# Performance work log

Hardware: AMD Instinct MI355X
Metric: run time of the kernel (lower is better)

The kernel has to match this reference:

```python
import jax, jax.numpy as jnp
import numpy as np
import math

B, T, D, NH, HD = 2, 1024, 768, 12, 64
V, L, E, CAP_F, H = 50257, 2, 8, 1.25, 2048
AUX_W, Z_W, THETA, EPS = 0.01, 0.001, 10000.0, 1e-5
N = B * T
CAP = int(math.ceil(N / E * CAP_F))  # 320


def setup_inputs():
    key = jax.random.key(0)
    ks = jax.random.split(key, 8)
    s = 0.02
    return dict(
        idx=jax.random.randint(ks[0], (B, T), 0, V),
        wte=jax.random.normal(ks[1], (V, D), jnp.float32) * s,
        wqkv=jax.random.normal(ks[2], (L, D, 3 * D), jnp.float32) * s,
        q_norm_w=jnp.ones((L, D), jnp.float32),
        k_norm_w=jnp.ones((L, D), jnp.float32),
        o_proj=jax.random.normal(ks[3], (L, D, D), jnp.float32) * s,
        ffn_norm_w=jnp.ones((L, D), jnp.float32),
        gate_w=jax.random.normal(ks[4], (L, D, E), jnp.float32) * s,
        w13=jax.random.normal(ks[5], (L, E, D, 2 * H), jnp.float32) * s,
        w2=jax.random.normal(ks[6], (L, E, H, D), jnp.float32) * s,
        ln_f_w=jnp.ones((D,), jnp.float32),
    )


def rmsnorm(x, w):
    return x * jax.lax.rsqrt(jnp.mean(x * x, axis=-1, keepdims=True) + EPS) * w


def rope(x, cos, sin):
    # x: (B, nh, T, HD) viewed as complex pairs on last dim
    xr = x.reshape(*x.shape[:-1], HD // 2, 2)
    x0, x1 = xr[..., 0], xr[..., 1]
    out = jnp.stack([x0 * cos - x1 * sin, x0 * sin + x1 * cos], axis=-1)
    return out.reshape(x.shape)


def moe(x, gate_w, w13, w2):
    # x: (B, T, D) -> Switch MoE (k=1) with capacity CAP and token drops
    x_flat = x.reshape(N, D).astype(jnp.float32)
    logits = x_flat @ gate_w  # (N, E) fp32
    probs = jax.nn.softmax(logits, axis=-1)
    top = jnp.argmax(logits, axis=-1)  # (N,)
    prob_mass = probs.mean(axis=0)
    fraction = jax.nn.one_hot(top, E, dtype=jnp.float32).mean(axis=0)
    balance_loss = jnp.sum(prob_mass * fraction) * AUX_W * E
    z = jax.nn.logsumexp(logits, axis=-1)
    z_loss = jnp.mean(z * z) * Z_W
    aux = balance_loss + z_loss

    sort_idx = jnp.argsort(top)  # stable
    sorted_assign = top[sort_idx]
    counts = jnp.bincount(sorted_assign, length=E)
    offsets = jnp.concatenate([jnp.zeros((1,), counts.dtype), jnp.cumsum(counts)])[:E]
    rank = jnp.arange(N) - offsets[sorted_assign]  # position within expert segment
    keep = rank < CAP
    x_perm = x_flat[sort_idx]
    slot = jnp.where(keep, rank, CAP)  # dropped -> overflow slot
    buf = jnp.zeros((E, CAP + 1, D), jnp.float32).at[sorted_assign, slot].set(x_perm)
    xb = buf[:, :CAP]  # (E, CAP, D)
    gu = jnp.einsum('ecd,edh->ech', xb, w13)  # (E, CAP, 2H)
    g, u = jnp.split(gu, 2, axis=-1)
    y = jnp.einsum('ech,ehd->ecd', jax.nn.silu(g) * u, w2)  # (E, CAP, D)
    out_perm = y[sorted_assign, jnp.minimum(rank, CAP - 1)] * keep[:, None]
    out_flat = jnp.zeros((N, D), jnp.float32).at[sort_idx].set(out_perm)
    return out_flat.reshape(B, T, D), aux, top.reshape(B, T), keep[jnp.argsort(sort_idx)].reshape(B, T)


def forward(idx, wte, wqkv, q_norm_w, k_norm_w, o_proj, ffn_norm_w, gate_w, w13, w2, ln_f_w):
    x = wte[idx]  # (B, T, D)
    freqs = 1.0 / (THETA ** (jnp.arange(0, HD, 2, dtype=jnp.float32) / HD))
    ang = jnp.outer(jnp.arange(T, dtype=jnp.float32), freqs)  # (T, HD//2)
    cos, sin = jnp.cos(ang)[None, None], jnp.sin(ang)[None, None]
    mask = jnp.where(jnp.tril(jnp.ones((T, T), bool)), 0.0, -jnp.inf)
    aux_total = jnp.float32(0.0)
    for l in range(L):
        qkv = x @ wqkv[l]
        q, k, v = jnp.split(qkv, 3, axis=-1)
        q = rmsnorm(q, q_norm_w[l])
        k = rmsnorm(k, k_norm_w[l])
        q = q.reshape(B, T, NH, HD).transpose(0, 2, 1, 3)
        k = k.reshape(B, T, NH, HD).transpose(0, 2, 1, 3)
        v = v.reshape(B, T, NH, HD).transpose(0, 2, 1, 3)
        q, k = rope(q, cos, sin), rope(k, cos, sin)
        scores = jnp.einsum('bhqd,bhkd->bhqk', q, k) / math.sqrt(HD) + mask
        attn = jax.nn.softmax(scores, axis=-1)
        y = jnp.einsum('bhqk,bhkd->bhqd', attn, v).transpose(0, 2, 1, 3).reshape(B, T, D)
        h = x + y @ o_proj[l]
        ffn_in = rmsnorm(h, ffn_norm_w[l])
        moe_out, aux, _, _ = moe(ffn_in, gate_w[l], w13[l], w2[l])
        aux_total = aux_total + aux
        x = h + moe_out
    x = rmsnorm(x, ln_f_w)
    logits = x @ wte.T  # tied lm_head
    return logits, aux_total


def reference(idx, wte, wqkv, q_norm_w, k_norm_w, o_proj, ffn_norm_w, gate_w, w13, w2, ln_f_w):
    return forward(idx, wte, wqkv, q_norm_w, k_norm_w, o_proj, ffn_norm_w, gate_w, w13, w2, ln_f_w)
```

## Files before the change

### kernel.cpp

```cpp
#include <hip/hip_runtime.h>

typedef __attribute__((ext_vector_type(8))) _Float16 half8;
typedef __attribute__((ext_vector_type(4))) float f32x4;

constexpr int Bc = 2, Tc = 1024, Dc = 768, NHc = 12, HDc = 64;
constexpr int Vc = 50257, Lc = 2, Ec = 8, Hc = 2048;
constexpr int Ntok = Bc * Tc;
constexpr int CAPc = 320, CAPPc = 384;
constexpr long long LOGITS_N = (long long)Bc * Tc * Vc;

typedef const __attribute__((address_space(1))) unsigned int* gas_t;
typedef __attribute__((address_space(3))) unsigned int* las_t;
__device__ __forceinline__ void gload16(const void* g, void* l) {
  __builtin_amdgcn_global_load_lds((gas_t)g, (las_t)l, 16, 0, 0);
}

__device__ __forceinline__ void splitf16(float a, unsigned short& h, unsigned short& l) {
  _Float16 hh = (_Float16)a;
  _Float16 ll = (_Float16)(a - (float)hh);
  h = __builtin_bit_cast(unsigned short, hh);
  l = __builtin_bit_cast(unsigned short, ll);
}
__device__ __forceinline__ unsigned short f16o(float a) {
  _Float16 hh = (_Float16)a;
  return __builtin_bit_cast(unsigned short, hh);
}


__global__ void embed_k(const int* __restrict__ idx, const float* __restrict__ wte,
                        float* __restrict__ x, unsigned short* __restrict__ x16,
                        float* __restrict__ psum, float* __restrict__ z2) {
  int n = blockIdx.x;
  int t = threadIdx.x;
  if (n == 0) {
    if (t < Lc * Ec) psum[t] = 0.f;
    if (t >= 32 && t < 32 + Lc) z2[t - 32] = 0.f;
  }
  long long v = idx[n];
  const float4* src = (const float4*)(wte + v * 768);
  float4* dst = (float4*)(x + (long long)n * 768);
  if (t < 192) {
    float4 val = src[t];
    dst[t] = val;
    ushort4 h, l;
    splitf16(val.x, h.x, l.x); splitf16(val.y, h.y, l.y);
    splitf16(val.z, h.z, l.z); splitf16(val.w, h.w, l.w);
    unsigned short* d = x16 + (long long)n * 1536 + t * 4;
    *(ushort4*)d = h;
    *(ushort4*)(d + 768) = l;
  }
}

__global__ void f2h4(const float* __restrict__ in, unsigned short* __restrict__ out,
                     long long n4) {
  long long i = (long long)blockIdx.x * 256 + threadIdx.x;
  if (i >= n4) return;
  float4 v = ((const float4*)in)[i];
  ushort4 o;
  o.x = f16o(v.x); o.y = f16o(v.y); o.z = f16o(v.z); o.w = f16o(v.w);
  ((ushort4*)out)[i] = o;
}

template <int SP, int ILV>
__global__ void __launch_bounds__(256) split2_wT(const float* __restrict__ src,
    unsigned short* __restrict__ dst, int K, int N, long long sS, long long sD) {
  __shared__ float t[32][33];
  int z = blockIdx.z;
  src += (long long)z * sS;
  dst += (long long)z * sD;
  int n0 = blockIdx.x * 32, k0 = blockIdx.y * 32;
  int tid = threadIdx.x;
  int r = tid >> 3, c4 = (tid & 7) * 4;
  float4 v = *(const float4*)(src + (long long)(k0 + r) * N + n0 + c4);
  t[r][c4 + 0] = v.x; t[r][c4 + 1] = v.y; t[r][c4 + 2] = v.z; t[r][c4 + 3] = v.w;
  __syncthreads();
  int n = tid >> 3, kq = (tid & 7) * 4;
  ushort4 h, l;
  splitf16(t[kq + 0][n], h.x, l.x);
  splitf16(t[kq + 1][n], h.y, l.y);
  splitf16(t[kq + 2][n], h.z, l.z);
  splitf16(t[kq + 3][n], h.w, l.w);
  const int lda = SP ? 2 * K : K;
  int nd = n0 + n;
  if (ILV) {
    int hh = nd & 2047, iu = nd >> 11;
    nd = ((hh >> 4) << 5) + (iu << 4) + (hh & 15);
  }
  unsigned short* d = dst + (long long)nd * lda + k0 + kq;
  *(ushort4*)d = h;
  if (SP) *(ushort4*)(d + K) = l;
}

__global__ void __launch_bounds__(256) rmsnorm_k(const float* in, int istride,
                                                 float* outp, int ostride,
                                                 const float* w) {
  long long n = blockIdx.x;
  const float* xr = in + n * istride;
  float* yr = outp + n * ostride;
  int tid = threadIdx.x;
  float s = 0.f;
  for (int i = tid; i < 768; i += 256) { float v = xr[i]; s += v * v; }
  #pragma unroll
  for (int o = 32; o; o >>= 1) s += __shfl_down(s, o);
  __shared__ float red[4];
  __shared__ float bs;
  if ((tid & 63) == 0) red[tid >> 6] = s;
  __syncthreads();
  if (tid == 0) bs = rsqrtf((red[0] + red[1] + red[2] + red[3]) / 768.0f + 1e-5f);
  __syncthreads();
  float sc = bs;
  for (int i = tid; i < 768; i += 256) yr[i] = xr[i] * sc * w[i];
}

__global__ void __launch_bounds__(256) rmsnorm_h(const float* in,
                                                 unsigned short* outp, const float* w) {
  long long n = blockIdx.x;
  const float* xr = in + n * 768;
  unsigned short* yr = outp + n * 768;
  int tid = threadIdx.x;
  float s = 0.f;
  for (int i = tid; i < 768; i += 256) { float v = xr[i]; s += v * v; }
  #pragma unroll
  for (int o = 32; o; o >>= 1) s += __shfl_down(s, o);
  __shared__ float red[4];
  __shared__ float bs;
  if ((tid & 63) == 0) red[tid >> 6] = s;
  __syncthreads();
  if (tid == 0) bs = rsqrtf((red[0] + red[1] + red[2] + red[3]) / 768.0f + 1e-5f);
  __syncthreads();
  float sc = bs;
  for (int i = tid; i < 768; i += 256) yr[i] = f16o(xr[i] * sc * w[i]);
}

__global__ void __launch_bounds__(256) qk_rope(const float* __restrict__ qkv,
    const float* __restrict__ qnw, const float* __restrict__ knw,
    unsigned short* __restrict__ qr, unsigned short* __restrict__ kr,
    unsigned short* __restrict__ vr) {
  int n = blockIdx.x;
  int t = n & 1023, b = n >> 10;
  const float* row = qkv + (long long)n * 2304;
  int tid = threadIdx.x;
  float sq = 0.f, sk = 0.f;
  for (int i = tid; i < 768; i += 256) {
    float q = row[i]; sq += q * q;
    float k = row[768 + i]; sk += k * k;
  }
  #pragma unroll
  for (int o = 32; o; o >>= 1) { sq += __shfl_down(sq, o); sk += __shfl_down(sk, o); }
  __shared__ float redq[4], redk[4];
  __shared__ float bq, bk;
  if ((tid & 63) == 0) { redq[tid >> 6] = sq; redk[tid >> 6] = sk; }
  __syncthreads();
  if (tid == 0) {
    bq = rsqrtf((redq[0] + redq[1] + redq[2] + redq[3]) / 768.0f + 1e-5f);
    bk = rsqrtf((redk[0] + redk[1] + redk[2] + redk[3]) / 768.0f + 1e-5f);
  }
  __syncthreads();
  float nq = bq, nk = bk;
  for (int i = tid; i < 384; i += 256) {
    int hh = i >> 5, j = i & 31;
    int c = hh * 64 + 2 * j;
    float ang = (float)t * powf(10000.0f, -((float)j * (1.0f / 32.0f)));
    float cs = cosf(ang), sn = sinf(ang);
    int z = b * 12 + hh;
    long long qb = ((long long)z * 1024 + t) * 128 + 2 * j;
    unsigned short h0, l0, h1, l1;
    float q0 = row[c] * nq * qnw[c], q1 = row[c + 1] * nq * qnw[c + 1];
    splitf16(q0 * cs - q1 * sn, h0, l0);
    splitf16(q0 * sn + q1 * cs, h1, l1);
    *(unsigned int*)&qr[qb] = (unsigned)h0 | ((unsigned)h1 << 16);
    *(unsigned int*)&qr[qb + 64] = (unsigned)l0 | ((unsigned)l1 << 16);
    float k0 = row[768 + c] * nk * knw[c], k1 = row[768 + c + 1] * nk * knw[c + 1];
    splitf16(k0 * cs - k1 * sn, h0, l0);
    splitf16(k0 * sn + k1 * cs, h1, l1);
    *(unsigned int*)&kr[qb] = (unsigned)h0 | ((unsigned)h1 << 16);
    *(unsigned int*)&kr[qb + 64] = (unsigned)l0 | ((unsigned)l1 << 16);
    splitf16(row[1536 + c], h0, l0);
    splitf16(row[1536 + c + 1], h1, l1);
    long long vb = ((long long)z * 64 + 2 * j) * 2048 + t;
    vr[vb] = h0; vr[vb + 1024] = l0;
    vr[vb + 2048] = h1; vr[vb + 3072] = l1;
  }
}

__global__ void __launch_bounds__(256) flash_attn(
    const unsigned short* __restrict__ qr, const unsigned short* __restrict__ kr,
    const unsigned short* __restrict__ vr, unsigned short* __restrict__ yout) {
  __shared__ __align__(16) unsigned short Ph[4][16][72];
  __shared__ __align__(16) unsigned short Pl[4][16][72];
  int bid = blockIdx.x;
  int z = bid >> 4;
  int qt = 15 - (bid & 15);
  int b = z / 12, h = z % 12;
  int q0 = qt * 64;
  int wave = threadIdx.x >> 6, lane = threadIdx.x & 63;
  int lr = lane & 15, lg = lane >> 4;
  int qw = q0 + wave * 16;
  half8 af[2][2];
  const unsigned short* qbase = qr + ((long long)z * 1024 + qw + lr) * 128;
  #pragma unroll
  for (int ks = 0; ks < 2; ++ks)
    #pragma unroll
    for (int p = 0; p < 2; ++p)
      af[ks][p] = *(const half8*)(qbase + p * 64 + ks * 32 + lg * 8);
  f32x4 accy[4];
  #pragma unroll
  for (int df = 0; df < 4; ++df) accy[df] = (f32x4){0.f, 0.f, 0.f, 0.f};
  float mrun[4] = {-3.4e38f, -3.4e38f, -3.4e38f, -3.4e38f};
  float srun[4] = {0.f, 0.f, 0.f, 0.f};
  for (int kt = 0; kt <= qt; ++kt) {
    int kv0 = kt * 64;
    f32x4 s[4];
    #pragma unroll
    for (int nf = 0; nf < 4; ++nf) s[nf] = (f32x4){0.f, 0.f, 0.f, 0.f};
    const unsigned short* kbase = kr + ((long long)z * 1024 + kv0 + lr) * 128;
    #pragma unroll
    for (int nf = 0; nf < 4; ++nf) {
      const unsigned short* kb = kbase + nf * 16 * 128;
      #pragma unroll
      for (int ks = 0; ks < 2; ++ks) {
        half8 bh = *(const half8*)(kb + ks * 32 + lg * 8);
        half8 bl = *(const half8*)(kb + 64 + ks * 32 + lg * 8);
        s[nf] = __builtin_amdgcn_mfma_f32_16x16x32_f16(af[ks][0], bh, s[nf], 0, 0, 0);
        s[nf] = __builtin_amdgcn_mfma_f32_16x16x32_f16(af[ks][1], bh, s[nf], 0, 0, 0);
        s[nf] = __builtin_amdgcn_mfma_f32_16x16x32_f16(af[ks][0], bl, s[nf], 0, 0, 0);
      }
    }
    bool diag = (kt == qt);
    #pragma unroll
    for (int nf = 0; nf < 4; ++nf)
      #pragma unroll
      for (int j = 0; j < 4; ++j) {
        float v = s[nf][j] * 0.125f;
        if (diag && (nf * 16 + lr > wave * 16 + lg * 4 + j)) v = -1e30f;
        s[nf][j] = v;
      }
    #pragma unroll
    for (int j = 0; j < 4; ++j) {
      float tm = fmaxf(fmaxf(s[0][j], s[1][j]), fmaxf(s[2][j], s[3][j]));
      #pragma unroll
      for (int o = 1; o < 16; o <<= 1) tm = fmaxf(tm, __shfl_xor(tm, o));
      float mnew = fmaxf(mrun[j], tm);
      float sc = expf(mrun[j] - mnew);
      float ts = 0.f;
      #pragma unroll
      for (int nf = 0; nf < 4; ++nf) {
        float p = expf(s[nf][j] - mnew);
        ts += p;
        unsigned short ph, pl;
        splitf16(p, ph, pl);
        Ph[wave][lg * 4 + j][nf * 16 + lr] = ph;
        Pl[wave][lg * 4 + j][nf * 16 + lr] = pl;
      }
      #pragma unroll
      for (int o = 1; o < 16; o <<= 1) ts += __shfl_xor(ts, o);
      srun[j] = srun[j] * sc + ts;
      mrun[j] = mnew;
      #pragma unroll
      for (int df = 0; df < 4; ++df) accy[df][j] *= sc;
    }
    #pragma unroll
    for (int ks2 = 0; ks2 < 2; ++ks2) {
      half8 aph = *(const half8*)&Ph[wave][lr][ks2 * 32 + lg * 8];
      half8 apl = *(const half8*)&Pl[wave][lr][ks2 * 32 + lg * 8];
      #pragma unroll
      for (int df = 0; df < 4; ++df) {
        const unsigned short* vb =
            vr + ((long long)z * 64 + df * 16 + lr) * 2048 + kv0 + ks2 * 32 + lg * 8;
        half8 bvh = *(const half8*)vb;
        half8 bvl = *(const half8*)(vb + 1024);
        accy[df] = __builtin_amdgcn_mfma_f32_16x16x32_f16(aph, bvh, accy[df], 0, 0, 0);
        accy[df] = __builtin_amdgcn_mfma_f32_16x16x32_f16(apl, bvh, accy[df], 0, 0, 0);
        accy[df] = __builtin_amdgcn_mfma_f32_16x16x32_f16(aph, bvl, accy[df], 0, 0, 0);
      }
    }
  }
  float inv[4];
  #pragma unroll
  for (int j = 0; j < 4; ++j) inv[j] = 1.0f / srun[j];
  #pragma unroll
  for (int df = 0; df < 4; ++df)
    #pragma unroll
    for (int j = 0; j < 4; ++j) {
      long long tok = (long long)b * 1024 + qw + lg * 4 + j;
      int col = h * 64 + df * 16 + lr;
      unsigned short hh, ll;
      splitf16(accy[df][j] * inv[j], hh, ll);
      yout[tok * 1536 + col] = hh;
      yout[tok * 1536 + 768 + col] = ll;
    }
}

__global__ void __launch_bounds__(256) gate_k(const float* __restrict__ xin,
    const float* __restrict__ gw, int* __restrict__ top,
    float* __restrict__ psum, float* __restrict__ z2) {
  __shared__ float gws[768 * 8];
  __shared__ float pacc[8];
  __shared__ float zacc;
  int tid = threadIdx.x;
  for (int i = tid; i < 768 * 8 / 4; i += 256) ((float4*)gws)[i] = ((const float4*)gw)[i];
  if (tid < 8) pacc[tid] = 0.f;
  if (tid == 0) zacc = 0.f;
  __syncthreads();
  int n = blockIdx.x * 256 + tid;
  const float4* xr4 = (const float4*)(xin + (long long)n * 768);
  float l[8] = {0, 0, 0, 0, 0, 0, 0, 0};
  for (int d4 = 0; d4 < 192; ++d4) {
    float4 xv = xr4[d4];
    const float* g = &gws[d4 * 32];
    #pragma unroll
    for (int e = 0; e < 8; ++e)
      l[e] += xv.x * g[e] + xv.y * g[8 + e] + xv.z * g[16 + e] + xv.w * g[24 + e];
  }
  float mx = l[0]; int bi = 0;
  #pragma unroll
  for (int e = 1; e < 8; ++e) if (l[e] > mx) { mx = l[e]; bi = e; }
  float p[8]; float se = 0.f;
  #pragma unroll
  for (int e = 0; e < 8; ++e) { p[e] = expf(l[e] - mx); se += p[e]; }
  float z = mx + logf(se);
  top[n] = bi;
  #pragma unroll
  for (int e = 0; e < 8; ++e) atomicAdd(&pacc[e], p[e] / se);
  atomicAdd(&zacc, z * z);
  __syncthreads();
  if (tid < 8) atomicAdd(&psum[tid], pacc[tid]);
  if (tid == 0) atomicAdd(z2, zacc);
}

__global__ void route_scan(const int* __restrict__ top, int* __restrict__ rank,
                           int* __restrict__ cnt) {
  int lane = threadIdx.x;
  int c[8] = {0, 0, 0, 0, 0, 0, 0, 0};
  unsigned long long below = (1ull << lane) - 1ull;
  for (int s = 0; s < Ntok / 64; ++s) {
    int n = s * 64 + lane;
    int e = top[n];
    int r = 0;
    #pragma unroll
    for (int q = 0; q < 8; ++q) {
      unsigned long long m = __ballot(e == q);
      if (e == q) r = c[q] + __popcll(m & below);
      c[q] += __popcll(m);
    }
    rank[n] = r;
  }
  #pragma unroll
  for (int q = 0; q < 8; ++q) if (lane == q) cnt[q] = c[q];
}

template <int SP>
__global__ void scatter_xb(const float* __restrict__ xin, const int* __restrict__ top,
                           const int* __restrict__ rank, unsigned short* __restrict__ xb) {
  int n = blockIdx.x;
  int r = rank[n];
  if (r >= CAPc) return;
  int e = top[n];
  int t = threadIdx.x;
  if (t >= 192) return;
  float4 v = ((const float4*)(xin + (long long)n * 768))[t];
  ushort4 h, l;
  splitf16(v.x, h.x, l.x); splitf16(v.y, h.y, l.y);
  splitf16(v.z, h.z, l.z); splitf16(v.w, h.w, l.w);
  const int lda = SP ? 1536 : 768;
  unsigned short* dst = xb + ((long long)e * CAPPc + r) * lda + t * 4;
  *(ushort4*)dst = h;
  if (SP) *(ushort4*)(dst + 768) = l;
}

__global__ void gather_add(const float* __restrict__ h, const float* __restrict__ yexp,
                           const int* __restrict__ top, const int* __restrict__ rank,
                           float* __restrict__ xo, unsigned short* __restrict__ x16) {
  int n = blockIdx.x;
  int r = rank[n], e = top[n];
  bool kept = r < CAPc;
  int rc = kept ? r : (CAPc - 1);
  const float4* hs = (const float4*)(h + (long long)n * 768);
  const float4* ys = (const float4*)(yexp + ((long long)e * CAPPc + rc) * 768);
  float4* dst = (float4*)(xo + (long long)n * 768);
  int t = threadIdx.x;
  if (t < 192) {
    float4 v = hs[t];
    if (kept) { float4 y = ys[t]; v.x += y.x; v.y += y.y; v.z += y.z; v.w += y.w; }
    dst[t] = v;
    ushort4 hh, ll;
    splitf16(v.x, hh.x, ll.x); splitf16(v.y, hh.y, ll.y);
    splitf16(v.z, hh.z, ll.z); splitf16(v.w, hh.w, ll.w);
    unsigned short* d = x16 + (long long)n * 1536 + t * 4;
    *(ushort4*)d = hh;
    *(ushort4*)(d + 768) = ll;
  }
}

__global__ void aux_fin(const float* __restrict__ psum, const int* __restrict__ cnt,
                        const float* __restrict__ z2, float* __restrict__ outp) {
  if (threadIdx.x == 0) {
    float aux = 0.f;
    for (int l = 0; l < Lc; ++l) {
      float bl = 0.f;
      for (int e = 0; e < 8; ++e)
        bl += (psum[l * 8 + e] * (1.0f / 2048.0f)) * ((float)cnt[l * 8 + e] * (1.0f / 2048.0f));
      aux += bl * (0.01f * 8.0f) + (z2[l] * (1.0f / 2048.0f)) * 0.001f;
    }
    outp[0] = aux;
  }
}

template <int BN, int SPLIT, int ADD, int NTAIL, int SILU>
__global__ void __launch_bounds__(256) gemm_h(
    const unsigned short* __restrict__ A, const unsigned short* __restrict__ Bt,
    float* __restrict__ C, const float* __restrict__ Add,
    int M, int N, int K, int ldc, int gx, int gy,
    long long sA, long long sB, int zdiv, long long sC1, long long sC2) {
  constexpr int FN = (BN == 128) ? 4 : 2;
  constexpr int APL = 128 * 32;
  constexpr int BPL = BN * 32;
  constexpr int BUF = 2 * APL + 2 * BPL;
  __shared__ __align__(16) unsigned short lds[2][BUF];
  int tot = gridDim.x;
  int lin = blockIdx.x;
  if ((tot & 7) == 0) lin = (lin & 7) * (tot >> 3) + (lin >> 3);
  int pz = lin / (gx * gy);
  int r2 = lin - pz * (gx * gy);
  const int m0 = (r2 % gx) * 128, n0 = (r2 / gx) * BN;
  A += (long long)pz * sA;
  Bt += (long long)pz * sB;
  const long long co = (long long)(pz / zdiv) * sC1 + (long long)(pz % zdiv) * sC2;
  const int lda = SPLIT ? 2 * K : K;
  const int NS = SPLIT ? K / 32 : K / 64;
  const int tid = threadIdx.x;
  const int lane = tid & 63, wave = tid >> 6;
  const int wm = (BN == 128) ? (wave >> 1) : (wave & 1);
  const int wn = (BN == 128) ? (wave & 1) : (wave >> 1);
  const int srow = tid >> 2, scol = (tid & 3) * 8;
  const unsigned short* Ar = A + (long long)(m0 + srow) * lda + scol;
  int br0 = n0 + srow;
  if (NTAIL) br0 = min(br0, N - 1);
  const unsigned short* Br = Bt + (long long)br0 * lda + scol;
  int br1 = n0 + srow + 64;
  if (NTAIL) br1 = min(br1, N - 1);
  const unsigned short* Br2 = Bt + (long long)br1 * lda + scol;

  auto STAGE = [&](int buf, int s) {
    const int kh = SPLIT ? s * 32 : s * 64;
    const int kl = SPLIT ? K + s * 32 : s * 64 + 32;
    unsigned short* L = lds[buf];
    gload16(Ar + kh, &L[wave * 512]);
    gload16(Ar + (long long)64 * lda + kh, &L[2048 + wave * 512]);
    gload16(Ar + kl, &L[APL + wave * 512]);
    gload16(Ar + (long long)64 * lda + kl, &L[APL + 2048 + wave * 512]);
    gload16(Br + kh, &L[2 * APL + wave * 512]);
    gload16(Br + kl, &L[2 * APL + BPL + wave * 512]);
    if (BN == 128) {
      gload16(Br2 + kh, &L[2 * APL + 2048 + wave * 512]);
      gload16(Br2 + kl, &L[2 * APL + BPL + 2048 + wave * 512]);
    }
  };

  f32x4 acc[4][FN];
  #pragma unroll
  for (int m = 0; m < 4; ++m)
    #pragma unroll
    for (int n = 0; n < FN; ++n) acc[m][n] = (f32x4){0.f, 0.f, 0.f, 0.f};

  STAGE(0, 0);
  int cur = 0;
  for (int s = 0; s < NS; ++s) {
    asm volatile("s_waitcnt vmcnt(0)" ::: "memory");
    __builtin_amdgcn_sched_barrier(0);
    __builtin_amdgcn_s_barrier();
    if (s + 1 < NS) STAGE(cur ^ 1, s + 1);
    const unsigned short* L = lds[cur];
    half8 bfh[FN], bfl[FN];
    #pragma unroll
    for (int n = 0; n < FN; ++n) {
      int bo = (wn * (FN * 16) + n * 16 + (lane & 15)) * 32 + (lane >> 4) * 8;
      bfh[n] = *(const half8*)&L[2 * APL + bo];
      bfl[n] = *(const half8*)&L[2 * APL + BPL + bo];
    }
    __builtin_amdgcn_s_setprio(1);
    #pragma unroll
    for (int m = 0; m < 4; ++m) {
      int ao = (wm * 64 + m * 16 + (lane & 15)) * 32 + (lane >> 4) * 8;
      half8 afh = *(const half8*)&L[ao];
      half8 afl = *(const half8*)&L[APL + ao];
      #pragma unroll
      for (int n = 0; n < FN; ++n) {
        acc[m][n] = __builtin_amdgcn_mfma_f32_16x16x32_f16(afh, bfh[n], acc[m][n], 0, 0, 0);
        if (SPLIT) {
          acc[m][n] = __builtin_amdgcn_mfma_f32_16x16x32_f16(afl, bfh[n], acc[m][n], 0, 0, 0);
          acc[m][n] = __builtin_amdgcn_mfma_f32_16x16x32_f16(afh, bfl[n], acc[m][n], 0, 0, 0);
        } else {
          acc[m][n] = __builtin_amdgcn_mfma_f32_16x16x32_f16(afl, bfl[n], acc[m][n], 0, 0, 0);
        }
      }
    }
    __builtin_amdgcn_s_setprio(0);
    cur ^= 1;
  }
  if constexpr (SILU) {
    unsigned short* act = (unsigned short*)C;
    #pragma unroll
    for (int m = 0; m < 4; ++m)
      #pragma unroll
      for (int p = 0; p < FN / 2; ++p) {
        f32x4 g = acc[m][2 * p], u = acc[m][2 * p + 1];
        int colh = ((n0 + wn * (FN * 16)) >> 1) + p * 16 + (lane & 15);
        #pragma unroll
        for (int j = 0; j < 4; ++j) {
          long long row = m0 + wm * 64 + m * 16 + (lane >> 4) * 4 + j;
          float gv = g[j];
          float a = gv / (1.f + expf(-gv)) * u[j];
          long long o = co + row * ldc + colh;
          if (SILU == 1) {
            unsigned short hh, ll;
            splitf16(a, hh, ll);
            act[o] = hh;
            act[o + 2048] = ll;
          } else {
            act[o] = f16o(a);
          }
        }
      }
  } else {
    #pragma unroll
    for (int m = 0; m < 4; ++m)
      #pragma unroll
      for (int n = 0; n < FN; ++n) {
        int col = n0 + wn * (FN * 16) + n * 16 + (lane & 15);
        if (!NTAIL || col < N) {
          #pragma unroll
          for (int j = 0; j < 4; ++j) {
            long long row = m0 + wm * 64 + m * 16 + (lane >> 4) * 4 + j;
            long long o = co + row * ldc + col;
            float v = acc[m][n][j];
            if (ADD) v += Add[o];
            C[o] = v;
          }
        }
      }
  }
}

__global__ void __launch_bounds__(512) gemm_logits(
    const unsigned short* __restrict__ A, const unsigned short* __restrict__ Bt,
    float* __restrict__ C, int M, int N, int K, int ldc, int gx) {
  constexpr int BUFS = 24576;
  constexpr int BOFF = 16384;
  __shared__ __align__(16) unsigned short lds[3 * BUFS];
  int tot = gridDim.x;
  int lin = blockIdx.x;
  if ((tot & 7) == 0) lin = (lin & 7) * (tot >> 3) + (lin >> 3);
  const int m0 = (lin % gx) * 256, n0 = (lin / gx) * 128;
  const int tid = threadIdx.x;
  const int lane = tid & 63;
  const int wm = (tid >> 6) >> 1, wn = (tid >> 6) & 1;
  const int NS = K / 64;

  auto STAGE = [&](int buf, int t) {
    const int k0 = t * 64;
    unsigned short* L = lds + buf * BUFS;
    #pragma unroll
    for (int i = 0; i < 4; ++i) {
      int idx = tid + i * 512;
      int row = idx >> 3, blk = idx & 7;
      gload16(A + (long long)(m0 + row) * K + k0 + ((blk ^ (row & 7)) << 3),
              L + idx * 8);
    }
    #pragma unroll
    for (int i = 0; i < 2; ++i) {
      int idx = tid + i * 512;
      int row = idx >> 3, blk = idx & 7;
      int br = min(n0 + row, N - 1);
      gload16(Bt + (long long)br * K + k0 + ((blk ^ (row & 7)) << 3),
              L + BOFF + idx * 8);
    }
  };

  f32x4 acc[4][4];
  #pragma unroll
  for (int mf = 0; mf < 4; ++mf)
    #pragma unroll
    for (int nf = 0; nf < 4; ++nf) acc[mf][nf] = (f32x4){0.f, 0.f, 0.f, 0.f};

  STAGE(0, 0); STAGE(1, 1);
  for (int s = 0; s < NS; ++s) {
    if (s + 1 < NS) asm volatile("s_waitcnt vmcnt(6)" ::: "memory");
    else            asm volatile("s_waitcnt vmcnt(0)" ::: "memory");
    __builtin_amdgcn_sched_barrier(0);
    __builtin_amdgcn_s_barrier();
    if (s + 2 < NS) STAGE((s + 2) % 3, s + 2);
    const unsigned short* L = lds + (s % 3) * BUFS;
    half8 a[4][2], b[4][2];
    #pragma unroll
    for (int mf = 0; mf < 4; ++mf)
      #pragma unroll
      for (int ks = 0; ks < 2; ++ks) {
        int row = wm * 64 + mf * 16 + (lane & 15);
        int blk = (ks * 4 + (lane >> 4)) ^ (row & 7);
        a[mf][ks] = *(const half8*)(L + row * 64 + blk * 8);
      }
    #pragma unroll
    for (int nf = 0; nf < 4; ++nf)
      #pragma unroll
      for (int ks = 0; ks < 2; ++ks) {
        int row = wn * 64 + nf * 16 + (lane & 15);
        int blk = (ks * 4 + (lane >> 4)) ^ (row & 7);
        b[nf][ks] = *(const half8*)(L + BOFF + row * 64 + blk * 8);
      }
    __builtin_amdgcn_s_setprio(1);
    #pragma unroll
    for (int ks = 0; ks < 2; ++ks)
      #pragma unroll
      for (int mf = 0; mf < 4; ++mf)
        #pragma unroll
        for (int nf = 0; nf < 4; ++nf)
          acc[mf][nf] = __builtin_amdgcn_mfma_f32_16x16x32_f16(a[mf][ks], b[nf][ks],
                                                               acc[mf][nf], 0, 0, 0);
    __builtin_amdgcn_s_setprio(0);
  }
  #pragma unroll
  for (int mf = 0; mf < 4; ++mf)
    #pragma unroll
    for (int nf = 0; nf < 4; ++nf) {
      int col = n0 + wn * 64 + nf * 16 + (lane & 15);
      if (col < N) {
        #pragma unroll
        for (int j = 0; j < 4; ++j) {
          long long row = m0 + wm * 64 + mf * 16 + (lane >> 4) * 4 + j;
          C[row * (long long)ldc + col] = acc[mf][nf][j];
        }
      }
    }
}


extern "C" void kernel_launch(void* const* d_in, const int* in_sizes, int n_in,
                              void* d_out, int out_size, void* d_ws, size_t ws_size,
                              hipStream_t stream) {
  (void)in_sizes; (void)n_in; (void)out_size; (void)ws_size;
  const int*   idx   = (const int*)d_in[0];
  const float* wte   = (const float*)d_in[1];
  const float* wqkv  = (const float*)d_in[2];
  const float* qnw   = (const float*)d_in[3];
  const float* knw   = (const float*)d_in[4];
  const float* oproj = (const float*)d_in[5];
  const float* ffnw  = (const float*)d_in[6];
  const float* gatew = (const float*)d_in[7];
  const float* w13   = (const float*)d_in[8];
  const float* w2p   = (const float*)d_in[9];
  const float* lnf   = (const float*)d_in[10];
  float* out = (float*)d_out;

  char* base = (char*)d_ws;
  size_t off = 0;
  auto alloc = [&](size_t bytes) -> char* {
    off = (off + 255) & ~(size_t)255;
    char* p = base + off; off += bytes; return p;
  };
  float* x     = (float*)alloc((size_t)Ntok * 768 * 4);
  float* qkv   = (float*)alloc((size_t)Ntok * 2304 * 4);
  float* hbuf  = (float*)alloc((size_t)Ntok * 768 * 4);
  float* ffn   = (float*)alloc((size_t)Ntok * 768 * 4);
  unsigned short* x16   = (unsigned short*)alloc((size_t)Ntok * 1536 * 2);
  unsigned short* yfl16 = (unsigned short*)alloc((size_t)Ntok * 1536 * 2);
  unsigned short* qr16  = (unsigned short*)alloc((size_t)24 * 1024 * 128 * 2);
  unsigned short* kr16  = (unsigned short*)alloc((size_t)24 * 1024 * 128 * 2);
  unsigned short* vr16  = (unsigned short*)alloc((size_t)24 * 64 * 2048 * 2);
  unsigned short* xb16  = (unsigned short*)alloc((size_t)Ec * CAPPc * 1536 * 2);
  unsigned short* wo16  = (unsigned short*)alloc((size_t)768 * 1536 * 2);
  unsigned short* xf16  = (unsigned short*)alloc((size_t)Ntok * 768 * 2);
  char* spb = alloc((size_t)24 * 1024 * 1024 * 4);
  float* yexp = (float*)spb;
  unsigned short* act16 = (unsigned short*)(spb + 50331648);
  unsigned short* wq16  = (unsigned short*)(spb + 75497472);
  unsigned short* w13_16 = (unsigned short*)alloc((size_t)Ec * 4096 * 1536 * 2);
  unsigned short* wt16   = w13_16;
  unsigned short* w2_16  = (unsigned short*)alloc((size_t)Ec * 768 * 4096 * 2);
  int* top    = (int*)alloc(Ntok * 4);
  int* rankb  = (int*)alloc(Ntok * 4);
  int* cnt    = (int*)alloc(Lc * Ec * 4);
  float* psum = (float*)alloc(Lc * Ec * 4);
  float* z2   = (float*)alloc(Lc * 4);

  embed_k<<<Ntok, 192, 0, stream>>>(idx, wte, x, x16, psum, z2);

  for (int l = 0; l < Lc; ++l) {
    split2_wT<1, 0><<<dim3(72, 24, 1), 256, 0, stream>>>(wqkv + (size_t)l * 768 * 2304,
                                                         wq16, 768, 2304, 0, 0);
    split2_wT<1, 0><<<dim3(24, 24, 1), 256, 0, stream>>>(oproj + (size_t)l * 768 * 768,
                                                         wo16, 768, 768, 0, 0);
    if (l == 0) {
      split2_wT<1, 1><<<dim3(128, 24, 8), 256, 0, stream>>>(w13, w13_16,
          768, 4096, (long long)768 * 4096, (long long)4096 * 1536);
      split2_wT<1, 0><<<dim3(24, 64, 8), 256, 0, stream>>>(w2p, w2_16,
          2048, 768, (long long)2048 * 768, (long long)768 * 4096);
    } else {
      split2_wT<0, 1><<<dim3(128, 24, 8), 256, 0, stream>>>(w13 + (size_t)Ec * 768 * 4096,
          w13_16, 768, 4096, (long long)768 * 4096, (long long)4096 * 768);
      split2_wT<0, 0><<<dim3(24, 64, 8), 256, 0, stream>>>(w2p + (size_t)Ec * 2048 * 768,
          w2_16, 2048, 768, (long long)2048 * 768, (long long)768 * 2048);
    }
    gemm_h<128, 1, 0, 0, 0><<<288, 256, 0, stream>>>(
        x16, wq16, qkv, nullptr, 2048, 2304, 768, 2304, 16, 18, 0, 0, 1, 0, 0);
    qk_rope<<<Ntok, 256, 0, stream>>>(qkv, qnw + l * 768, knw + l * 768, qr16, kr16, vr16);
    flash_attn<<<384, 256, 0, stream>>>(qr16, kr16, vr16, yfl16);
    gemm_h<64, 1, 1, 0, 0><<<192, 256, 0, stream>>>(
        yfl16, wo16, hbuf, x, 2048, 768, 768, 768, 16, 12, 0, 0, 1, 0, 0);
    rmsnorm_k<<<Ntok, 256, 0, stream>>>(hbuf, 768, ffn, 768, ffnw + l * 768);
    gate_k<<<Ntok / 256, 256, 0, stream>>>(ffn, gatew + (size_t)l * 768 * 8, top,
                                           psum + l * 8, z2 + l);
    route_scan<<<1, 64, 0, stream>>>(top, rankb, cnt + l * 8);
    if (l == 0) {
      scatter_xb<1><<<Ntok, 192, 0, stream>>>(ffn, top, rankb, xb16);
      gemm_h<128, 1, 0, 0, 1><<<768, 256, 0, stream>>>(
          xb16, w13_16, (float*)act16, nullptr, 384, 4096, 768, 4096, 3, 32,
          (long long)384 * 1536, (long long)4096 * 1536, 1, (long long)384 * 4096, 0);
      gemm_h<64, 1, 0, 0, 0><<<288, 256, 0, stream>>>(
          act16, w2_16, yexp, nullptr, 384, 768, 2048, 768, 3, 12,
          (long long)384 * 4096, (long long)768 * 4096, 1, (long long)384 * 768, 0);
    } else {
      scatter_xb<0><<<Ntok, 192, 0, stream>>>(ffn, top, rankb, xb16);
      gemm_h<128, 0, 0, 0, 2><<<768, 256, 0, stream>>>(
          xb16, w13_16, (float*)act16, nullptr, 384, 4096, 768, 2048, 3, 32,
          (long long)384 * 768, (long long)4096 * 768, 1, (long long)384 * 2048, 0);
      gemm_h<64, 0, 0, 0, 0><<<288, 256, 0, stream>>>(
          act16, w2_16, yexp, nullptr, 384, 768, 2048, 768, 3, 12,
          (long long)384 * 2048, (long long)768 * 2048, 1, (long long)384 * 768, 0);
    }
    gather_add<<<Ntok, 192, 0, stream>>>(hbuf, yexp, top, rankb, x, x16);
  }

  rmsnorm_h<<<Ntok, 256, 0, stream>>>(x, xf16, lnf);
  f2h4<<<(int)(((long long)Vc * 768 / 4 + 255) / 256), 256, 0, stream>>>(
      wte, wt16, (long long)Vc * 768 / 4);
  gemm_logits<<<8 * 393, 512, 0, stream>>>(xf16, wt16, out, 2048, Vc, 768, Vc, 8);
  aux_fin<<<1, 64, 0, stream>>>(psum, cnt, z2, out + LOGITS_N);
}
```

Before: 1.244 ms.

## Fuse FFN rmsnorm into gate/scatter, merge final prep kernels, fold aux into logits

Removes the separate FFN rmsnorm kernel and its fp32 intermediate buffer. The gate kernel now computes per-token rms scale (one wave per token) and applies the norm weight inline, storing the scale for scatter_xb to reuse. The final rmsnorm and the wte fp16 conversion are merged into one launch, the aux-loss finalizer is folded into the logits GEMM's first block, and the logits tile ordering is swapped to m-major. This reduces launch count and memory traffic, but the gate kernel's wave-per-token layout changes how its parallel work is shaped.

```diff
diff --git a/kernel.cpp b/kernel.cpp
--- a/kernel.cpp
+++ b/kernel.cpp
@@ -51,14 +51,35 @@
   }
 }
 
-__global__ void f2h4(const float* __restrict__ in, unsigned short* __restrict__ out,
-                     long long n4) {
-  long long i = (long long)blockIdx.x * 256 + threadIdx.x;
-  if (i >= n4) return;
-  float4 v = ((const float4*)in)[i];
-  ushort4 o;
-  o.x = f16o(v.x); o.y = f16o(v.y); o.z = f16o(v.z); o.w = f16o(v.w);
-  ((ushort4*)out)[i] = o;
+__global__ void __launch_bounds__(256) final_prep(const float* __restrict__ x,
+    const float* __restrict__ lnw, unsigned short* __restrict__ xf,
+    const float* __restrict__ wte, unsigned short* __restrict__ wt) {
+  int tid = threadIdx.x;
+  if (blockIdx.x < Ntok) {
+    long long n = blockIdx.x;
+    const float* xr = x + n * 768;
+    unsigned short* yr = xf + n * 768;
+    float s = 0.f;
+    for (int i = tid; i < 768; i += 256) { float v = xr[i]; s += v * v; }
+    #pragma unroll
+    for (int o = 32; o; o >>= 1) s += __shfl_down(s, o);
+    __shared__ float red[4];
+    __shared__ float bs;
+    if ((tid & 63) == 0) red[tid >> 6] = s;
+    __syncthreads();
+    if (tid == 0) bs = rsqrtf((red[0] + red[1] + red[2] + red[3]) / 768.0f + 1e-5f);
+    __syncthreads();
+    float sc = bs;
+    for (int i = tid; i < 768; i += 256) yr[i] = f16o(xr[i] * sc * lnw[i]);
+  } else {
+    long long i = (long long)(blockIdx.x - Ntok) * 256 + tid;
+    const long long n4 = (long long)Vc * 768 / 4;
+    if (i >= n4) return;
+    float4 v = ((const float4*)wte)[i];
+    ushort4 o;
+    o.x = f16o(v.x); o.y = f16o(v.y); o.z = f16o(v.z); o.w = f16o(v.w);
+    ((ushort4*)wt)[i] = o;
+  }
 }
 
 template <int SP, int ILV>
@@ -89,47 +110,6 @@
   unsigned short* d = dst + (long long)nd * lda + k0 + kq;
   *(ushort4*)d = h;
   if (SP) *(ushort4*)(d + K) = l;
-}
-
-__global__ void __launch_bounds__(256) rmsnorm_k(const float* in, int istride,
-                                                 float* outp, int ostride,
-                                                 const float* w) {
-  long long n = blockIdx.x;
-  const float* xr = in + n * istride;
-  float* yr = outp + n * ostride;
-  int tid = threadIdx.x;
-  float s = 0.f;
-  for (int i = tid; i < 768; i += 256) { float v = xr[i]; s += v * v; }
-  #pragma unroll
-  for (int o = 32; o; o >>= 1) s += __shfl_down(s, o);
-  __shared__ float red[4];
-  __shared__ float bs;
-  if ((tid & 63) == 0) red[tid >> 6] = s;
-  __syncthreads();
-  if (tid == 0) bs = rsqrtf((red[0] + red[1] + red[2] + red[3]) / 768.0f + 1e-5f);
-  __syncthreads();
-  float sc = bs;
-  for (int i = tid; i < 768; i += 256) yr[i] = xr[i] * sc * w[i];
-}
-
-__global__ void __launch_bounds__(256) rmsnorm_h(const float* in,
-                                                 unsigned short* outp, const float* w) {
-  long long n = blockIdx.x;
-  const float* xr = in + n * 768;
-  unsigned short* yr = outp + n * 768;
-  int tid = threadIdx.x;
-  float s = 0.f;
-  for (int i = tid; i < 768; i += 256) { float v = xr[i]; s += v * v; }
-  #pragma unroll
-  for (int o = 32; o; o >>= 1) s += __shfl_down(s, o);
-  __shared__ float red[4];
-  __shared__ float bs;
-  if ((tid & 63) == 0) red[tid >> 6] = s;
-  __syncthreads();
-  if (tid == 0) bs = rsqrtf((red[0] + red[1] + red[2] + red[3]) / 768.0f + 1e-5f);
-  __syncthreads();
-  float sc = bs;
-  for (int i = tid; i < 768; i += 256) yr[i] = f16o(xr[i] * sc * w[i]);
 }
 
 __global__ void __launch_bounds__(256) qk_rope(const float* __restrict__ qkv,
@@ -291,38 +271,60 @@
     }
 }
 
-__global__ void __launch_bounds__(256) gate_k(const float* __restrict__ xin,
-    const float* __restrict__ gw, int* __restrict__ top,
+__global__ void __launch_bounds__(256) gate_k(const float* __restrict__ h,
+    const float* __restrict__ w, const float* __restrict__ gw,
+    int* __restrict__ top, float* __restrict__ rsq,
     float* __restrict__ psum, float* __restrict__ z2) {
-  __shared__ float gws[768 * 8];
+  __shared__ float gws[8][772];
   __shared__ float pacc[8];
   __shared__ float zacc;
   int tid = threadIdx.x;
-  for (int i = tid; i < 768 * 8 / 4; i += 256) ((float4*)gws)[i] = ((const float4*)gw)[i];
+  for (int i = tid; i < 768 * 8; i += 256) {
+    int d = i >> 3, e = i & 7;
+    gws[e][d] = gw[i];
+  }
   if (tid < 8) pacc[tid] = 0.f;
   if (tid == 0) zacc = 0.f;
   __syncthreads();
-  int n = blockIdx.x * 256 + tid;
-  const float4* xr4 = (const float4*)(xin + (long long)n * 768);
+  int wave = tid >> 6, lane = tid & 63;
+  int n = blockIdx.x * 4 + wave;
+  const float* row = h + (long long)n * 768;
+  float ss = 0.f;
   float l[8] = {0, 0, 0, 0, 0, 0, 0, 0};
-  for (int d4 = 0; d4 < 192; ++d4) {
-    float4 xv = xr4[d4];
-    const float* g = &gws[d4 * 32];
+  #pragma unroll
+  for (int c = 0; c < 3; ++c) {
+    int i = c * 256 + lane * 4;
+    float4 v = *(const float4*)(row + i);
+    ss += v.x * v.x + v.y * v.y + v.z * v.z + v.w * v.w;
+    float4 wv = *(const float4*)(w + i);
+    float tx = v.x * wv.x, ty = v.y * wv.y, tz = v.z * wv.z, tw = v.w * wv.w;
     #pragma unroll
     for (int e = 0; e < 8; ++e)
-      l[e] += xv.x * g[e] + xv.y * g[8 + e] + xv.z * g[16 + e] + xv.w * g[24 + e];
-  }
-  float mx = l[0]; int bi = 0;
-  #pragma unroll
-  for (int e = 1; e < 8; ++e) if (l[e] > mx) { mx = l[e]; bi = e; }
-  float p[8]; float se = 0.f;
-  #pragma unroll
-  for (int e = 0; e < 8; ++e) { p[e] = expf(l[e] - mx); se += p[e]; }
-  float z = mx + logf(se);
-  top[n] = bi;
-  #pragma unroll
-  for (int e = 0; e < 8; ++e) atomicAdd(&pacc[e], p[e] / se);
-  atomicAdd(&zacc, z * z);
+      l[e] += tx * gws[e][i] + ty * gws[e][i + 1] + tz * gws[e][i + 2] + tw * gws[e][i + 3];
+  }
+  #pragma unroll
+  for (int o = 32; o; o >>= 1) {
+    ss += __shfl_down(ss, o);
+    #pragma unroll
+    for (int e = 0; e < 8; ++e) l[e] += __shfl_down(l[e], o);
+  }
+  if (lane == 0) {
+    float rs = rsqrtf(ss / 768.0f + 1e-5f);
+    rsq[n] = rs;
+    #pragma unroll
+    for (int e = 0; e < 8; ++e) l[e] *= rs;
+    float mx = l[0]; int bi = 0;
+    #pragma unroll
+    for (int e = 1; e < 8; ++e) if (l[e] > mx) { mx = l[e]; bi = e; }
+    float p[8]; float se = 0.f;
+    #pragma unroll
+    for (int e = 0; e < 8; ++e) { p[e] = expf(l[e] - mx); se += p[e]; }
+    float z = mx + logf(se);
+    top[n] = bi;
+    #pragma unroll
+    for (int e = 0; e < 8; ++e) atomicAdd(&pacc[e], p[e] / se);
+    atomicAdd(&zacc, z * z);
+  }
   __syncthreads();
   if (tid < 8) atomicAdd(&psum[tid], pacc[tid]);
   if (tid == 0) atomicAdd(z2, zacc);
@@ -350,22 +352,26 @@
 }
 
 template <int SP>
-__global__ void scatter_xb(const float* __restrict__ xin, const int* __restrict__ top,
+__global__ void scatter_xb(const float* __restrict__ h, const float* __restrict__ w,
+                           const float* __restrict__ rsq, const int* __restrict__ top,
                            const int* __restrict__ rank, unsigned short* __restrict__ xb) {
   int n = blockIdx.x;
   int r = rank[n];
   if (r >= CAPc) return;
   int e = top[n];
+  float rs = rsq[n];
   int t = threadIdx.x;
   if (t >= 192) return;
-  float4 v = ((const float4*)(xin + (long long)n * 768))[t];
-  ushort4 h, l;
-  splitf16(v.x, h.x, l.x); splitf16(v.y, h.y, l.y);
-  splitf16(v.z, h.z, l.z); splitf16(v.w, h.w, l.w);
+  float4 v = ((const float4*)(h + (long long)n * 768))[t];
+  float4 wv = ((const float4*)w)[t];
+  v.x *= rs * wv.x; v.y *= rs * wv.y; v.z *= rs * wv.z; v.w *= rs * wv.w;
+  ushort4 hh, ll;
+  splitf16(v.x, hh.x, ll.x); splitf16(v.y, hh.y, ll.y);
+  splitf16(v.z, hh.z, ll.z); splitf16(v.w, hh.w, ll.w);
   const int lda = SP ? 1536 : 768;
   unsigned short* dst = xb + ((long long)e * CAPPc + r) * lda + t * 4;
-  *(ushort4*)dst = h;
-  if (SP) *(ushort4*)(dst + 768) = l;
+  *(ushort4*)dst = hh;
+  if (SP) *(ushort4*)(dst + 768) = ll;
 }
 
 __global__ void gather_add(const float* __restrict__ h, const float* __restrict__ yexp,
@@ -389,20 +395,6 @@
     unsigned short* d = x16 + (long long)n * 1536 + t * 4;
     *(ushort4*)d = hh;
     *(ushort4*)(d + 768) = ll;
-  }
-}
-
-__global__ void aux_fin(const float* __restrict__ psum, const int* __restrict__ cnt,
-                        const float* __restrict__ z2, float* __restrict__ outp) {
-  if (threadIdx.x == 0) {
-    float aux = 0.f;
-    for (int l = 0; l < Lc; ++l) {
-      float bl = 0.f;
-      for (int e = 0; e < 8; ++e)
-        bl += (psum[l * 8 + e] * (1.0f / 2048.0f)) * ((float)cnt[l * 8 + e] * (1.0f / 2048.0f));
-      aux += bl * (0.01f * 8.0f) + (z2[l] * (1.0f / 2048.0f)) * 0.001f;
-    }
-    outp[0] = aux;
   }
 }
 
@@ -544,14 +536,26 @@
 
 __global__ void __launch_bounds__(512) gemm_logits(
     const unsigned short* __restrict__ A, const unsigned short* __restrict__ Bt,
-    float* __restrict__ C, int M, int N, int K, int ldc, int gx) {
+    float* __restrict__ C, int M, int N, int K, int ldc, int gyn,
+    const float* __restrict__ psum, const int* __restrict__ cnt,
+    const float* __restrict__ z2, float* __restrict__ auxout) {
   constexpr int BUFS = 24576;
   constexpr int BOFF = 16384;
   __shared__ __align__(16) unsigned short lds[3 * BUFS];
+  if (blockIdx.x == 0 && threadIdx.x == 0) {
+    float aux = 0.f;
+    for (int l = 0; l < Lc; ++l) {
+      float bl = 0.f;
+      for (int e = 0; e < 8; ++e)
+        bl += (psum[l * 8 + e] * (1.0f / 2048.0f)) * ((float)cnt[l * 8 + e] * (1.0f / 2048.0f));
+      aux += bl * (0.01f * 8.0f) + (z2[l] * (1.0f / 2048.0f)) * 0.001f;
+    }
+    auxout[0] = aux;
+  }
   int tot = gridDim.x;
   int lin = blockIdx.x;
   if ((tot & 7) == 0) lin = (lin & 7) * (tot >> 3) + (lin >> 3);
-  const int m0 = (lin % gx) * 256, n0 = (lin / gx) * 128;
+  const int m0 = (lin / gyn) * 256, n0 = (lin % gyn) * 128;
   const int tid = threadIdx.x;
   const int lane = tid & 63;
   const int wm = (tid >> 6) >> 1, wn = (tid >> 6) & 1;
@@ -661,7 +665,6 @@
   float* x     = (float*)alloc((size_t)Ntok * 768 * 4);
   float* qkv   = (float*)alloc((size_t)Ntok * 2304 * 4);
   float* hbuf  = (float*)alloc((size_t)Ntok * 768 * 4);
-  float* ffn   = (float*)alloc((size_t)Ntok * 768 * 4);
   unsigned short* x16   = (unsigned short*)alloc((size_t)Ntok * 1536 * 2);
   unsigned short* yfl16 = (unsigned short*)alloc((size_t)Ntok * 1536 * 2);
   unsigned short* qr16  = (unsigned short*)alloc((size_t)24 * 1024 * 128 * 2);
@@ -682,6 +685,7 @@
   int* cnt    = (int*)alloc(Lc * Ec * 4);
   float* psum = (float*)alloc(Lc * Ec * 4);
   float* z2   = (float*)alloc(Lc * 4);
+  float* rsq  = (float*)alloc(Ntok * 4);
 
   embed_k<<<Ntok, 192, 0, stream>>>(idx, wte, x, x16, psum, z2);
 
@@ -707,12 +711,12 @@
     flash_attn<<<384, 256, 0, stream>>>(qr16, kr16, vr16, yfl16);
     gemm_h<64, 1, 1, 0, 0><<<192, 256, 0, stream>>>(
         yfl16, wo16, hbuf, x, 2048, 768, 768, 768, 16, 12, 0, 0, 1, 0, 0);
-    rmsnorm_k<<<Ntok, 256, 0, stream>>>(hbuf, 768, ffn, 768, ffnw + l * 768);
-    gate_k<<<Ntok / 256, 256, 0, stream>>>(ffn, gatew + (size_t)l * 768 * 8, top,
-                                           psum + l * 8, z2 + l);
+    gate_k<<<Ntok / 4, 256, 0, stream>>>(hbuf, ffnw + l * 768,
+                                         gatew + (size_t)l * 768 * 8, top, rsq,
+                                         psum + l * 8, z2 + l);
     route_scan<<<1, 64, 0, stream>>>(top, rankb, cnt + l * 8);
     if (l == 0) {
-      scatter_xb<1><<<Ntok, 192, 0, stream>>>(ffn, top, rankb, xb16);
+      scatter_xb<1><<<Ntok, 192, 0, stream>>>(hbuf, ffnw + l * 768, rsq, top, rankb, xb16);
       gemm_h<128, 1, 0, 0, 1><<<768, 256, 0, stream>>>(
           xb16, w13_16, (float*)act16, nullptr, 384, 4096, 768, 4096, 3, 32,
           (long long)384 * 1536, (long long)4096 * 1536, 1, (long long)384 * 4096, 0);
@@ -720,7 +724,7 @@
           act16, w2_16, yexp, nullptr, 384, 768, 2048, 768, 3, 12,
           (long long)384 * 4096, (long long)768 * 4096, 1, (long long)384 * 768, 0);
     } else {
-      scatter_xb<0><<<Ntok, 192, 0, stream>>>(ffn, top, rankb, xb16);
+      scatter_xb<0><<<Ntok, 192, 0, stream>>>(hbuf, ffnw + l * 768, rsq, top, rankb, xb16);
       gemm_h<128, 0, 0, 0, 2><<<768, 256, 0, stream>>>(
           xb16, w13_16, (float*)act16, nullptr, 384, 4096, 768, 2048, 3, 32,
           (long long)384 * 768, (long long)4096 * 768, 1, (long long)384 * 2048, 0);
@@ -731,9 +735,7 @@
     gather_add<<<Ntok, 192, 0, stream>>>(hbuf, yexp, top, rankb, x, x16);
   }
 
-  rmsnorm_h<<<Ntok, 256, 0, stream>>>(x, xf16, lnf);
-  f2h4<<<(int)(((long long)Vc * 768 / 4 + 255) / 256), 256, 0, stream>>>(
-      wte, wt16, (long long)Vc * 768 / 4);
-  gemm_logits<<<8 * 393, 512, 0, stream>>>(xf16, wt16, out, 2048, Vc, 768, Vc, 8);
-  aux_fin<<<1, 64, 0, stream>>>(psum, cnt, z2, out + LOGITS_N);
-}
+  final_prep<<<Ntok + 37694, 256, 0, stream>>>(x, lnf, xf16, wte, wt16);
+  gemm_logits<<<8 * 393, 512, 0, stream>>>(xf16, wt16, out, 2048, Vc, 768, Vc, 393,
+                                           psum, cnt, z2, out + LOGITS_N);
+}
```

Result: faster. 1.143 ms (-8.2%).
